# Optimization experiments

Hardware: AMD Instinct MI355X
Metric: run time of the kernel (lower is better)

## Reference

```python
import jax, jax.numpy as jnp
import numpy as np

N = 100000
E = 1600000
IN_C = 256
HID = 256
OUT_C = 10
G = 64  # number of graphs in batch


def setup_inputs() -> dict:
    key = jax.random.key(0)
    k1, k2, k3, k4, k5, k6, k7 = jax.random.split(key, 7)
    x = jax.random.normal(k1, (N, IN_C), dtype=jnp.float32)
    edge_index = jax.random.randint(k2, (2, E), 0, N, dtype=jnp.int64)
    batch = jnp.sort(jax.random.randint(k3, (N,), 0, G, dtype=jnp.int64))
    # GCNConv weight (glorot-ish) and bias
    W1 = jax.random.normal(k4, (IN_C, HID), dtype=jnp.float32) / np.sqrt(IN_C)
    b1 = jnp.zeros((HID,), dtype=jnp.float32)
    # final Linear
    W2 = jax.random.normal(k5, (HID, OUT_C), dtype=jnp.float32) / np.sqrt(HID)
    b2 = jax.random.normal(k6, (OUT_C,), dtype=jnp.float32) * 0.01
    return {"x": x, "edge_index": edge_index, "batch": batch,
            "W1": W1, "b1": b1, "W2": W2, "b2": b2}


def reference(x, edge_index, batch, W1, b1, W2, b2):
    # ---- GCNConv(in_channels, hidden_dim), add_self_loops=True, symmetric norm ----
    src = edge_index[0]
    dst = edge_index[1]
    loop = jnp.arange(N, dtype=src.dtype)
    src = jnp.concatenate([src, loop])  # [E+N]
    dst = jnp.concatenate([dst, loop])
    # degree on destination nodes (incl. self-loops) -> >= 1 everywhere
    deg = jax.ops.segment_sum(jnp.ones_like(dst, dtype=x.dtype), dst, num_segments=N)
    dinv = jax.lax.rsqrt(deg)  # deg >= 1, safe
    h = x @ W1  # linear transform first (PyG GCNConv order)
    norm = dinv[src] * dinv[dst]  # [E+N]
    msgs = h[src] * norm[:, None]  # gather + scale
    agg = jax.ops.segment_sum(msgs, dst, num_segments=N) + b1  # scatter-add + bias
    # ---- relu; dropout is identity in eval mode ----
    hrelu = jax.nn.relu(agg)
    # ---- global_mean_pool over batch ids ----
    sums = jax.ops.segment_sum(hrelu, batch, num_segments=G)
    counts = jax.ops.segment_sum(jnp.ones((N,), dtype=x.dtype), batch, num_segments=G)
    pooled = sums / jnp.maximum(counts, 1.0)[:, None]  # [G, HID]
    # ---- final linear ----
    return pooled @ W2 + b2
```

## Files before the change

### kernel.cpp

```cpp
#include <hip/hip_runtime.h>

#define NN 100000
#define EE 1600000
#define C 256
#define OUTC 10
#define NG 64

#define BSH 7
#define NBK 782
#define CHUNK 2048
#define NBLK1 ((EE + CHUNK - 1) / CHUNK)
#define PADSLACK 1024

#define NODES_PER_GROUP 8
#define NODES_PER_BLOCK 32
#define AGG_BLOCKS 3125
#define AGG_HALF 1563

#define PRE_CNT_BLKS 391
#define PRE_W1_BLKS 256

typedef __bf16 bf16x8 __attribute__((ext_vector_type(8)));
typedef float f32x4 __attribute__((ext_vector_type(4)));
typedef float f32x2 __attribute__((ext_vector_type(2)));

__device__ __forceinline__ int chan_logical(int p) {
    return ((p & 15) << 4) | (p >> 4);
}

__device__ __forceinline__ ushort f2bf(float f) {
    unsigned u = __float_as_uint(f);
    return (ushort)((u + 0x7fffu + ((u >> 16) & 1u)) >> 16);
}
__device__ __forceinline__ bf16x8 as_bf16x8(uint4 v) {
    union { uint4 u; bf16x8 b; } c; c.u = v; return c.b;
}

__device__ __forceinline__ void acc_fp8x4(float4& s, unsigned v) {
    f32x2 lo = __builtin_amdgcn_cvt_pk_f32_fp8(v, false);
    f32x2 hi = __builtin_amdgcn_cvt_pk_f32_fp8(v, true);
    s.x += lo[0]; s.y += lo[1]; s.z += hi[0]; s.w += hi[1];
}

__global__ __launch_bounds__(256) void pre_kernel(const int* __restrict__ ei,
                                                  int* __restrict__ bhist,
                                                  const int* __restrict__ batch,
                                                  float* __restrict__ cnt,
                                                  const float* __restrict__ W1,
                                                  ushort* __restrict__ w1f,
                                                  unsigned* __restrict__ gz) {
    __shared__ int h[NBK];
    const int bid = blockIdx.x;
    const int t = threadIdx.x;
    if (bid < NBLK1) {
        for (int i = t; i < NBK; i += 256) h[i] = 0;
        __syncthreads();
        const int base = bid * CHUNK;
        const int end = min(base + CHUNK, EE);
        for (int e = base + t; e < end; e += 256)
            atomicAdd(&h[ei[EE + e] >> BSH], 1);
        __syncthreads();
        for (int i = t; i < NBK; i += 256)
            if (h[i]) atomicAdd(&bhist[i], h[i]);
    } else if (bid < NBLK1 + PRE_CNT_BLKS) {
        if (t < NG) h[t] = 0;
        __syncthreads();
        int i = (bid - NBLK1) * 256 + t;
        if (i < NN) atomicAdd(&h[batch[i]], 1);
        __syncthreads();
        if (t < NG && h[t]) atomicAdd(&cnt[t], (float)h[t]);
    } else {
        int wb = bid - (NBLK1 + PRE_CNT_BLKS);
        int tt = wb * 256 + t;
        if (wb == 0 && t < 64) gz[t] = 0;
        int k = tt >> 8, n = tt & 255;
        int kb = k >> 5, q = (k >> 3) & 3, j = k & 7;
        int nt = n >> 4, ln = (n & 15) + q * 16;
        w1f[(size_t)(((kb * 16 + nt) * 64) + ln) * 8 + j] = f2bf(W1[tt]);
    }
}

__global__ __launch_bounds__(1024) void bucket_scan_kernel(const int* __restrict__ bhist,
                                                           int* __restrict__ bbase,
                                                           int* __restrict__ bcur) {
    __shared__ int sc[1024];
    const int t = threadIdx.x;
    int v = (t < NBK) ? bhist[t] : 0;
    sc[t] = v;
    __syncthreads();
    for (int off = 1; off < 1024; off <<= 1) {
        int tmp = (t >= off) ? sc[t - off] : 0;
        __syncthreads();
        sc[t] += tmp;
        __syncthreads();
    }
    int excl = sc[t] - v;
    if (t < NBK) { bbase[t] = excl; bcur[t] = excl; }
    if (t == NBK - 1) bbase[NBK] = sc[t];
}

__global__ __launch_bounds__(256) void bucket_scatter_kernel(const int* __restrict__ ei,
                                                             int* __restrict__ bcur,
                                                             unsigned* __restrict__ bmaj) {
    __shared__ int h[NBK];
    for (int t = threadIdx.x; t < NBK; t += 256) h[t] = 0;
    __syncthreads();
    const int base = blockIdx.x * CHUNK;
    const int end = min(base + CHUNK, EE);
    for (int e = base + threadIdx.x; e < end; e += 256)
        atomicAdd(&h[ei[EE + e] >> BSH], 1);
    __syncthreads();
    for (int t = threadIdx.x; t < NBK; t += 256) {
        int c = h[t];
        h[t] = c ? atomicAdd(&bcur[t], c) : 0;
    }
    __syncthreads();
    for (int e = base + threadIdx.x; e < end; e += 256) {
        int d = ei[EE + e];
        int s = ei[e];
        int b = d >> BSH;
        int p = atomicAdd(&h[b], 1);
        bmaj[p] = (unsigned)s | ((unsigned)(d & 127) << 17);
    }
}

__global__ __launch_bounds__(256) void bucket_csr_kernel(const unsigned* __restrict__ bmaj,
                                                         const int* __restrict__ bbase,
                                                         int* __restrict__ rowend,
                                                         float* __restrict__ dinv,
                                                         int* __restrict__ csrcol) {
    __shared__ int h[128];
    __shared__ int sc[128];
    __shared__ int cur[128];
    const int b = blockIdx.x;
    const int t = threadIdx.x;
    const int e0 = bbase[b], e1 = bbase[b + 1];
    const int region0 = ((e0 + 7) & ~7) + b * PADSLACK;
    if (t < 128) h[t] = 0;
    __syncthreads();
    for (int e = e0 + t; e < e1; e += 256)
        atomicAdd(&h[bmaj[e] >> 17], 1);
    __syncthreads();
    int deg = 0, pd = 0, node = 0;
    if (t < 128) {
        deg = h[t];
        node = b * 128 + t;
        pd = (node < NN) ? ((deg + 7) & ~7) : 0;
        sc[t] = pd;
    }
    __syncthreads();
    for (int off = 1; off < 128; off <<= 1) {
        int tmp = (t >= off && t < 128) ? sc[t - off] : 0;
        __syncthreads();
        if (t < 128) sc[t] += tmp;
        __syncthreads();
    }
    if (t < 128) {
        int pstart = region0 + sc[t] - pd;
        if (node < NN) {
            rowend[node] = pstart + pd;
            dinv[node] = rsqrtf((float)deg + 1.0f);
            for (int j = deg; j < pd; j++) csrcol[pstart + j] = NN;
        }
        cur[t] = pstart;
    }
    __syncthreads();
    for (int e = e0 + t; e < e1; e += 256) {
        unsigned v = bmaj[e];
        int p = atomicAdd(&cur[v >> 17], 1);
        csrcol[p] = (int)(v & 0x1FFFFu);
    }
}

__global__ __launch_bounds__(256, 2) void gemm_mfma_kernel(const float* __restrict__ x,
                                                           const ushort* __restrict__ w1f,
                                                           const float* __restrict__ dinv,
                                                           uchar* __restrict__ g) {
    const int lane = threadIdx.x & 63;
    const int wid = threadIdx.x >> 6;
    const int wave = blockIdx.x * 4 + wid;
    const int r0 = wave * 32;
    if (r0 >= NN) return;
    const int mrow = lane & 15;
    const int q = lane >> 4;

    f32x4 acc[2][16];
    #pragma unroll
    for (int mt = 0; mt < 2; mt++)
        #pragma unroll
        for (int nt = 0; nt < 16; nt++)
            acc[mt][nt] = (f32x4){0.f, 0.f, 0.f, 0.f};

    const float* xp0 = x + (size_t)(r0 + mrow) * C + q * 8;
    const float* xp1 = xp0 + (size_t)16 * C;
    const ushort* bp = w1f + (size_t)lane * 8;

    #pragma unroll 1
    for (int kb = 0; kb < 8; kb++) {
        const int ko = kb * 32;
        float4 a0lo = *(const float4*)(xp0 + ko);
        float4 a0hi = *(const float4*)(xp0 + ko + 4);
        float4 a1lo = *(const float4*)(xp1 + ko);
        float4 a1hi = *(const float4*)(xp1 + ko + 4);
        uint4 bbv[16];
        const ushort* bkb = bp + (size_t)kb * 16 * 512;
        #pragma unroll
        for (int nt = 0; nt < 16; nt++)
            bbv[nt] = *(const uint4*)(bkb + (size_t)nt * 512);

        bf16x8 a0, a1;
        a0[0] = (__bf16)a0lo.x; a0[1] = (__bf16)a0lo.y;
        a0[2] = (__bf16)a0lo.z; a0[3] = (__bf16)a0lo.w;
        a0[4] = (__bf16)a0hi.x; a0[5] = (__bf16)a0hi.y;
        a0[6] = (__bf16)a0hi.z; a0[7] = (__bf16)a0hi.w;
        a1[0] = (__bf16)a1lo.x; a1[1] = (__bf16)a1lo.y;
        a1[2] = (__bf16)a1lo.z; a1[3] = (__bf16)a1lo.w;
        a1[4] = (__bf16)a1hi.x; a1[5] = (__bf16)a1hi.y;
        a1[6] = (__bf16)a1hi.z; a1[7] = (__bf16)a1hi.w;

        #pragma unroll
        for (int nt = 0; nt < 16; nt++) {
            bf16x8 bb = as_bf16x8(bbv[nt]);
            acc[0][nt] = __builtin_amdgcn_mfma_f32_16x16x32_bf16(a0, bb, acc[0][nt], 0, 0, 0);
            acc[1][nt] = __builtin_amdgcn_mfma_f32_16x16x32_bf16(a1, bb, acc[1][nt], 0, 0, 0);
        }
    }

    #pragma unroll
    for (int mt = 0; mt < 2; mt++) {
        #pragma unroll
        for (int r = 0; r < 4; r++) {
            int row = r0 + mt * 16 + q * 4 + r;
            float dv = dinv[row];
            uint4 dw;
            unsigned t0, t1, t2, t3;
            t0 = __builtin_amdgcn_cvt_pk_fp8_f32(acc[mt][0][r] * dv,  acc[mt][1][r] * dv,  0,  false);
            dw.x = __builtin_amdgcn_cvt_pk_fp8_f32(acc[mt][2][r] * dv,  acc[mt][3][r] * dv,  t0, true);
            t1 = __builtin_amdgcn_cvt_pk_fp8_f32(acc[mt][4][r] * dv,  acc[mt][5][r] * dv,  0,  false);
            dw.y = __builtin_amdgcn_cvt_pk_fp8_f32(acc[mt][6][r] * dv,  acc[mt][7][r] * dv,  t1, true);
            t2 = __builtin_amdgcn_cvt_pk_fp8_f32(acc[mt][8][r] * dv,  acc[mt][9][r] * dv,  0,  false);
            dw.z = __builtin_amdgcn_cvt_pk_fp8_f32(acc[mt][10][r] * dv, acc[mt][11][r] * dv, t2, true);
            t3 = __builtin_amdgcn_cvt_pk_fp8_f32(acc[mt][12][r] * dv, acc[mt][13][r] * dv, 0,  false);
            dw.w = __builtin_amdgcn_cvt_pk_fp8_f32(acc[mt][14][r] * dv, acc[mt][15][r] * dv, t3, true);
            *(uint4*)(g + (size_t)row * C + mrow * 16) = dw;
        }
    }
}

__global__ __launch_bounds__(256) void agg_pool_kernel(const unsigned* __restrict__ g32,
                                                       const int* __restrict__ rowend,
                                                       const int* __restrict__ csrcol,
                                                       const int* __restrict__ bbase,
                                                       const float* __restrict__ dinv,
                                                       const float* __restrict__ b1,
                                                       const int* __restrict__ batch,
                                                       float* __restrict__ sums,
                                                       const int blk0) {
    const int lane = threadIdx.x & 63;
    const int wid = threadIdx.x >> 6;
    const int c4 = lane * 4;
    const int nodeA = (blockIdx.x + blk0) * NODES_PER_BLOCK + wid * NODES_PER_GROUP;
    float4 bv;
    bv.x = b1[chan_logical(c4 + 0)];
    bv.y = b1[chan_logical(c4 + 1)];
    bv.z = b1[chan_logical(c4 + 2)];
    bv.w = b1[chan_logical(c4 + 3)];
    const unsigned* gp = g32 + lane;

    int rprev;
    if ((nodeA & 127) == 0) {
        int b = nodeA >> BSH;
        rprev = ((bbase[b] + 7) & ~7) + b * PADSLACK;
    } else {
        rprev = rowend[nodeA - 1];
    }

    float4 pool = make_float4(0.f, 0.f, 0.f, 0.f);
    int curb = -1;
    #pragma unroll 1
    for (int i = nodeA; i < nodeA + NODES_PER_GROUP; i++) {
        int r1 = rowend[i];
        int r0 = rprev;
        rprev = r1;
        int bi = batch[i];
        if (bi != curb) {
            if (curb >= 0) {
                atomicAdd(&sums[curb * C + c4 + 0], pool.x);
                atomicAdd(&sums[curb * C + c4 + 1], pool.y);
                atomicAdd(&sums[curb * C + c4 + 2], pool.z);
                atomicAdd(&sums[curb * C + c4 + 3], pool.w);
            }
            curb = bi;
            pool = make_float4(0.f, 0.f, 0.f, 0.f);
        }
        float4 s = make_float4(0.f, 0.f, 0.f, 0.f);
        acc_fp8x4(s, gp[(size_t)i * 64]);
        #pragma unroll 1
        for (int e = r0; e < r1; e += 8) {
            int4 iv0 = *(const int4*)(csrcol + e);
            int4 iv1 = *(const int4*)(csrcol + e + 4);
            unsigned v0 = gp[(size_t)iv0.x * 64];
            unsigned v1 = gp[(size_t)iv0.y * 64];
            unsigned v2 = gp[(size_t)iv0.z * 64];
            unsigned v3 = gp[(size_t)iv0.w * 64];
            unsigned v4 = gp[(size_t)iv1.x * 64];
            unsigned v5 = gp[(size_t)iv1.y * 64];
            unsigned v6 = gp[(size_t)iv1.z * 64];
            unsigned v7 = gp[(size_t)iv1.w * 64];
            acc_fp8x4(s, v0); acc_fp8x4(s, v1); acc_fp8x4(s, v2); acc_fp8x4(s, v3);
            acc_fp8x4(s, v4); acc_fp8x4(s, v5); acc_fp8x4(s, v6); acc_fp8x4(s, v7);
        }
        float dv = dinv[i];
        pool.x += fmaxf(fmaf(dv, s.x, bv.x), 0.f);
        pool.y += fmaxf(fmaf(dv, s.y, bv.y), 0.f);
        pool.z += fmaxf(fmaf(dv, s.z, bv.z), 0.f);
        pool.w += fmaxf(fmaf(dv, s.w, bv.w), 0.f);
    }
    if (curb >= 0) {
        atomicAdd(&sums[curb * C + c4 + 0], pool.x);
        atomicAdd(&sums[curb * C + c4 + 1], pool.y);
        atomicAdd(&sums[curb * C + c4 + 2], pool.z);
        atomicAdd(&sums[curb * C + c4 + 3], pool.w);
    }
}

__global__ __launch_bounds__(256) void final_kernel(const float* __restrict__ sums,
                                                    const float* __restrict__ cnt,
                                                    const float* __restrict__ W2,
                                                    const float* __restrict__ b2,
                                                    float* __restrict__ out) {
    __shared__ float p[C];
    int gi = blockIdx.x;
    float cdiv = fmaxf(cnt[gi], 1.0f);
    p[threadIdx.x] = sums[gi * C + threadIdx.x] / cdiv;
    __syncthreads();
    if (threadIdx.x < OUTC) {
        float acc = b2[threadIdx.x];
        for (int k = 0; k < C; k++)
            acc += p[k] * W2[chan_logical(k) * OUTC + threadIdx.x];
        out[gi * OUTC + threadIdx.x] = acc;
    }
}

extern "C" void kernel_launch(void* const* d_in, const int* in_sizes, int n_in,
                              void* d_out, int out_size, void* d_ws, size_t ws_size,
                              hipStream_t stream) {
    const float* x     = (const float*)d_in[0];
    const int*   ei    = (const int*)d_in[1];
    const int*   batch = (const int*)d_in[2];
    const float* W1    = (const float*)d_in[3];
    const float* b1    = (const float*)d_in[4];
    const float* W2    = (const float*)d_in[5];
    const float* b2    = (const float*)d_in[6];
    float* out = (float*)d_out;

    char* w = (char*)d_ws;
    size_t off = 0;
    auto carve = [&](size_t bytes) {
        void* p = w + off;
        off = (off + bytes + 255) & ~(size_t)255;
        return p;
    };
    uchar*    g        = (uchar*)   carve((size_t)(NN + 1) * C);
    int*      rowend   = (int*)     carve((size_t)NN * 4);
    float*    dinv     = (float*)   carve((size_t)NN * 4);
    int*      csrcol   = (int*)     carve((size_t)(EE + (size_t)NBK * PADSLACK + 128) * 4);
    unsigned* bmaj     = (unsigned*)carve((size_t)EE * 4);
    int*      bbase    = (int*)     carve((size_t)(NBK + 1) * 4);
    int*      bcur     = (int*)     carve((size_t)NBK * 4);
    ushort*   w1f      = (ushort*)  carve((size_t)C * C * 2);
    int*      bhist    = (int*)     carve((size_t)NBK * 4);
    float*    sums     = (float*)   carve((size_t)NG * C * 4);
    float*    cnt      = (float*)   carve((size_t)NG * 4);
    size_t zero_bytes = (size_t)((char*)cnt + (size_t)NG * 4 - (char*)bhist);

    hipMemsetAsync(bhist, 0, zero_bytes, stream);

    pre_kernel<<<NBLK1 + PRE_CNT_BLKS + PRE_W1_BLKS, 256, 0, stream>>>(
        ei, bhist, batch, cnt, W1, w1f, (unsigned*)(g + (size_t)NN * C));
    bucket_scan_kernel<<<1, 1024, 0, stream>>>(bhist, bbase, bcur);
    bucket_scatter_kernel<<<NBLK1, 256, 0, stream>>>(ei, bcur, bmaj);
    bucket_csr_kernel<<<NBK, 256, 0, stream>>>(bmaj, bbase, rowend, dinv, csrcol);
    gemm_mfma_kernel<<<(NN / 32 + 3) / 4, 256, 0, stream>>>(x, w1f, dinv, g);
    agg_pool_kernel<<<AGG_HALF, 256, 0, stream>>>(
        (const unsigned*)g, rowend, csrcol, bbase, dinv, b1, batch, sums, 0);
    agg_pool_kernel<<<AGG_BLOCKS - AGG_HALF, 256, 0, stream>>>(
        (const unsigned*)g, rowend, csrcol, bbase, dinv, b1, batch, sums, AGG_HALF);
    final_kernel<<<NG, 256, 0, stream>>>(sums, cnt, W2, b2, out);
}
```

Before: 409.1 us.

## Replace two-level bucket sort CSR build with global degree count and atomic scatter

The CSR build no longer runs a bucket histogram, a bucket-major scatter and a per-bucket CSR pass. It now counts per-node degrees with global atomics, reduces and scans padded degrees per 256-node bucket, assigns row starts, and scatters edges straight into csrcol with per-node atomic cursors. This drops the intermediate bmaj array and one pass over the edges, at the cost of heavily contended global atomics and nondeterministic order within each row. The aggregation launch is also split into four launches instead of two.

```diff
diff --git a/kernel.cpp b/kernel.cpp
--- a/kernel.cpp
+++ b/kernel.cpp
@@ -6,16 +6,16 @@
 #define OUTC 10
 #define NG 64
 
-#define BSH 7
-#define NBK 782
-#define CHUNK 2048
-#define NBLK1 ((EE + CHUNK - 1) / CHUNK)
-#define PADSLACK 1024
+#define BSH 8
+#define NBK 391
+
+#define E4 (EE / 4)
+#define EBLK ((E4 + 255) / 256)
 
 #define NODES_PER_GROUP 8
 #define NODES_PER_BLOCK 32
 #define AGG_BLOCKS 3125
-#define AGG_HALF 1563
+#define AGG_Q 782
 
 #define PRE_CNT_BLKS 391
 #define PRE_W1_BLKS 256
@@ -43,34 +43,33 @@
 }
 
 __global__ __launch_bounds__(256) void pre_kernel(const int* __restrict__ ei,
-                                                  int* __restrict__ bhist,
+                                                  int* __restrict__ degcur,
                                                   const int* __restrict__ batch,
                                                   float* __restrict__ cnt,
                                                   const float* __restrict__ W1,
                                                   ushort* __restrict__ w1f,
                                                   unsigned* __restrict__ gz) {
-    __shared__ int h[NBK];
+    __shared__ int h[NG];
     const int bid = blockIdx.x;
     const int t = threadIdx.x;
-    if (bid < NBLK1) {
-        for (int i = t; i < NBK; i += 256) h[i] = 0;
-        __syncthreads();
-        const int base = bid * CHUNK;
-        const int end = min(base + CHUNK, EE);
-        for (int e = base + t; e < end; e += 256)
-            atomicAdd(&h[ei[EE + e] >> BSH], 1);
-        __syncthreads();
-        for (int i = t; i < NBK; i += 256)
-            if (h[i]) atomicAdd(&bhist[i], h[i]);
-    } else if (bid < NBLK1 + PRE_CNT_BLKS) {
+    if (bid < EBLK) {
+        int idx = bid * 256 + t;
+        if (idx < E4) {
+            int4 d4 = ((const int4*)(ei + EE))[idx];
+            atomicAdd(&degcur[d4.x], 1);
+            atomicAdd(&degcur[d4.y], 1);
+            atomicAdd(&degcur[d4.z], 1);
+            atomicAdd(&degcur[d4.w], 1);
+        }
+    } else if (bid < EBLK + PRE_CNT_BLKS) {
         if (t < NG) h[t] = 0;
         __syncthreads();
-        int i = (bid - NBLK1) * 256 + t;
+        int i = (bid - EBLK) * 256 + t;
         if (i < NN) atomicAdd(&h[batch[i]], 1);
         __syncthreads();
         if (t < NG && h[t]) atomicAdd(&cnt[t], (float)h[t]);
     } else {
-        int wb = bid - (NBLK1 + PRE_CNT_BLKS);
+        int wb = bid - (EBLK + PRE_CNT_BLKS);
         int tt = wb * 256 + t;
         if (wb == 0 && t < 64) gz[t] = 0;
         int k = tt >> 8, n = tt & 255;
@@ -80,96 +79,78 @@
     }
 }
 
-__global__ __launch_bounds__(1024) void bucket_scan_kernel(const int* __restrict__ bhist,
-                                                           int* __restrict__ bbase,
-                                                           int* __restrict__ bcur) {
-    __shared__ int sc[1024];
+__global__ __launch_bounds__(256) void bsum_kernel(const int* __restrict__ degcur,
+                                                   int* __restrict__ bsum) {
+    __shared__ int r[256];
+    const int b = blockIdx.x;
     const int t = threadIdx.x;
-    int v = (t < NBK) ? bhist[t] : 0;
+    int node = b * 256 + t;
+    int d = (node < NN) ? degcur[node] : 0;
+    r[t] = (d + 7) & ~7;
+    __syncthreads();
+    for (int off = 128; off > 0; off >>= 1) {
+        if (t < off) r[t] += r[t + off];
+        __syncthreads();
+    }
+    if (t == 0) bsum[b] = r[0];
+}
+
+__global__ __launch_bounds__(512) void bucket_scan_kernel(const int* __restrict__ bsum,
+                                                          int* __restrict__ bbase) {
+    __shared__ int sc[512];
+    const int t = threadIdx.x;
+    int v = (t < NBK) ? bsum[t] : 0;
     sc[t] = v;
     __syncthreads();
-    for (int off = 1; off < 1024; off <<= 1) {
+    for (int off = 1; off < 512; off <<= 1) {
         int tmp = (t >= off) ? sc[t - off] : 0;
         __syncthreads();
         sc[t] += tmp;
         __syncthreads();
     }
-    int excl = sc[t] - v;
-    if (t < NBK) { bbase[t] = excl; bcur[t] = excl; }
+    if (t < NBK) bbase[t] = sc[t] - v;
     if (t == NBK - 1) bbase[NBK] = sc[t];
 }
 
-__global__ __launch_bounds__(256) void bucket_scatter_kernel(const int* __restrict__ ei,
-                                                             int* __restrict__ bcur,
-                                                             unsigned* __restrict__ bmaj) {
-    __shared__ int h[NBK];
-    for (int t = threadIdx.x; t < NBK; t += 256) h[t] = 0;
-    __syncthreads();
-    const int base = blockIdx.x * CHUNK;
-    const int end = min(base + CHUNK, EE);
-    for (int e = base + threadIdx.x; e < end; e += 256)
-        atomicAdd(&h[ei[EE + e] >> BSH], 1);
-    __syncthreads();
-    for (int t = threadIdx.x; t < NBK; t += 256) {
-        int c = h[t];
-        h[t] = c ? atomicAdd(&bcur[t], c) : 0;
-    }
-    __syncthreads();
-    for (int e = base + threadIdx.x; e < end; e += 256) {
-        int d = ei[EE + e];
-        int s = ei[e];
-        int b = d >> BSH;
-        int p = atomicAdd(&h[b], 1);
-        bmaj[p] = (unsigned)s | ((unsigned)(d & 127) << 17);
-    }
-}
-
-__global__ __launch_bounds__(256) void bucket_csr_kernel(const unsigned* __restrict__ bmaj,
-                                                         const int* __restrict__ bbase,
-                                                         int* __restrict__ rowend,
-                                                         float* __restrict__ dinv,
-                                                         int* __restrict__ csrcol) {
-    __shared__ int h[128];
-    __shared__ int sc[128];
-    __shared__ int cur[128];
+__global__ __launch_bounds__(256) void csrlite_kernel(int* __restrict__ degcur,
+                                                      const int* __restrict__ bbase,
+                                                      int* __restrict__ rowend,
+                                                      float* __restrict__ dinv,
+                                                      int* __restrict__ csrcol) {
+    __shared__ int sc[256];
     const int b = blockIdx.x;
     const int t = threadIdx.x;
-    const int e0 = bbase[b], e1 = bbase[b + 1];
-    const int region0 = ((e0 + 7) & ~7) + b * PADSLACK;
-    if (t < 128) h[t] = 0;
+    int node = b * 256 + t;
+    int d = (node < NN) ? degcur[node] : 0;
+    int pd = (node < NN) ? ((d + 7) & ~7) : 0;
+    sc[t] = pd;
     __syncthreads();
-    for (int e = e0 + t; e < e1; e += 256)
-        atomicAdd(&h[bmaj[e] >> 17], 1);
-    __syncthreads();
-    int deg = 0, pd = 0, node = 0;
-    if (t < 128) {
-        deg = h[t];
-        node = b * 128 + t;
-        pd = (node < NN) ? ((deg + 7) & ~7) : 0;
-        sc[t] = pd;
-    }
-    __syncthreads();
-    for (int off = 1; off < 128; off <<= 1) {
-        int tmp = (t >= off && t < 128) ? sc[t - off] : 0;
-        __syncthreads();
-        if (t < 128) sc[t] += tmp;
-        __syncthreads();
-    }
-    if (t < 128) {
-        int pstart = region0 + sc[t] - pd;
-        if (node < NN) {
-            rowend[node] = pstart + pd;
-            dinv[node] = rsqrtf((float)deg + 1.0f);
-            for (int j = deg; j < pd; j++) csrcol[pstart + j] = NN;
-        }
-        cur[t] = pstart;
-    }
-    __syncthreads();
-    for (int e = e0 + t; e < e1; e += 256) {
-        unsigned v = bmaj[e];
-        int p = atomicAdd(&cur[v >> 17], 1);
-        csrcol[p] = (int)(v & 0x1FFFFu);
-    }
+    for (int off = 1; off < 256; off <<= 1) {
+        int tmp = (t >= off) ? sc[t - off] : 0;
+        __syncthreads();
+        sc[t] += tmp;
+        __syncthreads();
+    }
+    if (node < NN) {
+        int pstart = bbase[b] + sc[t] - pd;
+        rowend[node] = pstart + pd;
+        dinv[node] = rsqrtf((float)d + 1.0f);
+        for (int j = d; j < pd; j++) csrcol[pstart + j] = NN;
+        degcur[node] = pstart;
+    }
+}
+
+__global__ __launch_bounds__(256) void scatter_kernel(const int* __restrict__ ei,
+                                                      int* __restrict__ cur,
+                                                      int* __restrict__ csrcol) {
+    int idx = blockIdx.x * 256 + threadIdx.x;
+    if (idx >= E4) return;
+    int4 s4 = ((const int4*)ei)[idx];
+    int4 d4 = ((const int4*)(ei + EE))[idx];
+    int p0 = atomicAdd(&cur[d4.x], 1); csrcol[p0] = s4.x;
+    int p1 = atomicAdd(&cur[d4.y], 1); csrcol[p1] = s4.y;
+    int p2 = atomicAdd(&cur[d4.z], 1); csrcol[p2] = s4.z;
+    int p3 = atomicAdd(&cur[d4.w], 1); csrcol[p3] = s4.w;
 }
 
 __global__ __launch_bounds__(256, 2) void gemm_mfma_kernel(const float* __restrict__ x,
@@ -268,9 +249,8 @@
     const unsigned* gp = g32 + lane;
 
     int rprev;
-    if ((nodeA & 127) == 0) {
-        int b = nodeA >> BSH;
-        rprev = ((bbase[b] + 7) & ~7) + b * PADSLACK;
+    if ((nodeA & 255) == 0) {
+        rprev = bbase[nodeA >> BSH];
     } else {
         rprev = rowend[nodeA - 1];
     }
@@ -364,27 +344,31 @@
     uchar*    g        = (uchar*)   carve((size_t)(NN + 1) * C);
     int*      rowend   = (int*)     carve((size_t)NN * 4);
     float*    dinv     = (float*)   carve((size_t)NN * 4);
-    int*      csrcol   = (int*)     carve((size_t)(EE + (size_t)NBK * PADSLACK + 128) * 4);
-    unsigned* bmaj     = (unsigned*)carve((size_t)EE * 4);
+    int*      csrcol   = (int*)     carve((size_t)(EE + 8 * NN + 64) * 4);
+    int*      bsum     = (int*)     carve((size_t)NBK * 4);
     int*      bbase    = (int*)     carve((size_t)(NBK + 1) * 4);
-    int*      bcur     = (int*)     carve((size_t)NBK * 4);
     ushort*   w1f      = (ushort*)  carve((size_t)C * C * 2);
-    int*      bhist    = (int*)     carve((size_t)NBK * 4);
+    int*      degcur   = (int*)     carve((size_t)NN * 4);
     float*    sums     = (float*)   carve((size_t)NG * C * 4);
     float*    cnt      = (float*)   carve((size_t)NG * 4);
-    size_t zero_bytes = (size_t)((char*)cnt + (size_t)NG * 4 - (char*)bhist);
-
-    hipMemsetAsync(bhist, 0, zero_bytes, stream);
-
-    pre_kernel<<<NBLK1 + PRE_CNT_BLKS + PRE_W1_BLKS, 256, 0, stream>>>(
-        ei, bhist, batch, cnt, W1, w1f, (unsigned*)(g + (size_t)NN * C));
-    bucket_scan_kernel<<<1, 1024, 0, stream>>>(bhist, bbase, bcur);
-    bucket_scatter_kernel<<<NBLK1, 256, 0, stream>>>(ei, bcur, bmaj);
-    bucket_csr_kernel<<<NBK, 256, 0, stream>>>(bmaj, bbase, rowend, dinv, csrcol);
+    size_t zero_bytes = (size_t)((char*)cnt + (size_t)NG * 4 - (char*)degcur);
+
+    hipMemsetAsync(degcur, 0, zero_bytes, stream);
+
+    pre_kernel<<<EBLK + PRE_CNT_BLKS + PRE_W1_BLKS, 256, 0, stream>>>(
+        ei, degcur, batch, cnt, W1, w1f, (unsigned*)(g + (size_t)NN * C));
+    bsum_kernel<<<NBK, 256, 0, stream>>>(degcur, bsum);
+    bucket_scan_kernel<<<1, 512, 0, stream>>>(bsum, bbase);
+    csrlite_kernel<<<NBK, 256, 0, stream>>>(degcur, bbase, rowend, dinv, csrcol);
+    scatter_kernel<<<EBLK, 256, 0, stream>>>(ei, degcur, csrcol);
     gemm_mfma_kernel<<<(NN / 32 + 3) / 4, 256, 0, stream>>>(x, w1f, dinv, g);
-    agg_pool_kernel<<<AGG_HALF, 256, 0, stream>>>(
+    agg_pool_kernel<<<AGG_Q, 256, 0, stream>>>(
         (const unsigned*)g, rowend, csrcol, bbase, dinv, b1, batch, sums, 0);
-    agg_pool_kernel<<<AGG_BLOCKS - AGG_HALF, 256, 0, stream>>>(
-        (const unsigned*)g, rowend, csrcol, bbase, dinv, b1, batch, sums, AGG_HALF);
+    agg_pool_kernel<<<AGG_Q, 256, 0, stream>>>(
+        (const unsigned*)g, rowend, csrcol, bbase, dinv, b1, batch, sums, AGG_Q);
+    agg_pool_kernel<<<AGG_Q, 256, 0, stream>>>(
+        (const unsigned*)g, rowend, csrcol, bbase, dinv, b1, batch, sums, 2 * AGG_Q);
+    agg_pool_kernel<<<AGG_BLOCKS - 3 * AGG_Q, 256, 0, stream>>>(
+        (const unsigned*)g, rowend, csrcol, bbase, dinv, b1, batch, sums, 3 * AGG_Q);
     final_kernel<<<NG, 256, 0, stream>>>(sums, cnt, W2, b2, out);
 }
```

New measurement: 610.5 us. 1.49x slower.

## Replace atomic bucket cursors with per-chunk histograms and a column prefix scan

Applied to the files above, without the earlier changes.

The edge bucketing now stores a per-chunk histogram and computes each chunk's per-bucket offset with a new column-scan kernel. This removes the scatter kernel's second histogram pass and its global atomics on bucket cursors, and makes the scatter deterministic. Edge loads become int4 vector loads with a larger chunk size, and the aggregation launch is split into four pieces instead of two. The cost is an extra kernel launch and a strided 391x782 histogram read and write, while the scatter now runs with half as many blocks.

```diff
diff --git a/kernel.cpp b/kernel.cpp
--- a/kernel.cpp
+++ b/kernel.cpp
@@ -8,14 +8,16 @@
 
 #define BSH 7
 #define NBK 782
-#define CHUNK 2048
-#define NBLK1 ((EE + CHUNK - 1) / CHUNK)
+#define CHUNK 4096
+#define NCHUNK 391
+#define CI4 1024
+#define E4 (EE / 4)
 #define PADSLACK 1024
 
 #define NODES_PER_GROUP 8
 #define NODES_PER_BLOCK 32
 #define AGG_BLOCKS 3125
-#define AGG_HALF 1563
+#define AGG_Q 782
 
 #define PRE_CNT_BLKS 391
 #define PRE_W1_BLKS 256
@@ -43,7 +45,7 @@
 }
 
 __global__ __launch_bounds__(256) void pre_kernel(const int* __restrict__ ei,
-                                                  int* __restrict__ bhist,
+                                                  int* __restrict__ chunkhist,
                                                   const int* __restrict__ batch,
                                                   float* __restrict__ cnt,
                                                   const float* __restrict__ W1,
@@ -52,25 +54,30 @@
     __shared__ int h[NBK];
     const int bid = blockIdx.x;
     const int t = threadIdx.x;
-    if (bid < NBLK1) {
+    if (bid < NCHUNK) {
         for (int i = t; i < NBK; i += 256) h[i] = 0;
         __syncthreads();
-        const int base = bid * CHUNK;
-        const int end = min(base + CHUNK, EE);
-        for (int e = base + t; e < end; e += 256)
-            atomicAdd(&h[ei[EE + e] >> BSH], 1);
+        const int base4 = bid * CI4;
+        const int end4 = min(base4 + CI4, E4);
+        for (int i = base4 + t; i < end4; i += 256) {
+            int4 d4 = ((const int4*)(ei + EE))[i];
+            atomicAdd(&h[d4.x >> BSH], 1);
+            atomicAdd(&h[d4.y >> BSH], 1);
+            atomicAdd(&h[d4.z >> BSH], 1);
+            atomicAdd(&h[d4.w >> BSH], 1);
+        }
         __syncthreads();
         for (int i = t; i < NBK; i += 256)
-            if (h[i]) atomicAdd(&bhist[i], h[i]);
-    } else if (bid < NBLK1 + PRE_CNT_BLKS) {
+            chunkhist[bid * NBK + i] = h[i];
+    } else if (bid < NCHUNK + PRE_CNT_BLKS) {
         if (t < NG) h[t] = 0;
         __syncthreads();
-        int i = (bid - NBLK1) * 256 + t;
+        int i = (bid - NCHUNK) * 256 + t;
         if (i < NN) atomicAdd(&h[batch[i]], 1);
         __syncthreads();
         if (t < NG && h[t]) atomicAdd(&cnt[t], (float)h[t]);
     } else {
-        int wb = bid - (NBLK1 + PRE_CNT_BLKS);
+        int wb = bid - (NCHUNK + PRE_CNT_BLKS);
         int tt = wb * 256 + t;
         if (wb == 0 && t < 64) gz[t] = 0;
         int k = tt >> 8, n = tt & 255;
@@ -80,12 +87,29 @@
     }
 }
 
-__global__ __launch_bounds__(1024) void bucket_scan_kernel(const int* __restrict__ bhist,
-                                                           int* __restrict__ bbase,
-                                                           int* __restrict__ bcur) {
+__global__ __launch_bounds__(512) void rowscan_kernel(int* __restrict__ chunkhist,
+                                                      int* __restrict__ bsum) {
+    __shared__ int sc[512];
+    const int b = blockIdx.x;
+    const int t = threadIdx.x;
+    int v = (t < NCHUNK) ? chunkhist[t * NBK + b] : 0;
+    sc[t] = v;
+    __syncthreads();
+    for (int off = 1; off < 512; off <<= 1) {
+        int tmp = (t >= off) ? sc[t - off] : 0;
+        __syncthreads();
+        sc[t] += tmp;
+        __syncthreads();
+    }
+    if (t < NCHUNK) chunkhist[t * NBK + b] = sc[t] - v;
+    if (t == 511) bsum[b] = sc[511];
+}
+
+__global__ __launch_bounds__(1024) void bucket_scan_kernel(const int* __restrict__ bsum,
+                                                           int* __restrict__ bbase) {
     __shared__ int sc[1024];
     const int t = threadIdx.x;
-    int v = (t < NBK) ? bhist[t] : 0;
+    int v = (t < NBK) ? bsum[t] : 0;
     sc[t] = v;
     __syncthreads();
     for (int off = 1; off < 1024; off <<= 1) {
@@ -94,33 +118,33 @@
         sc[t] += tmp;
         __syncthreads();
     }
-    int excl = sc[t] - v;
-    if (t < NBK) { bbase[t] = excl; bcur[t] = excl; }
+    if (t < NBK) bbase[t] = sc[t] - v;
     if (t == NBK - 1) bbase[NBK] = sc[t];
 }
 
 __global__ __launch_bounds__(256) void bucket_scatter_kernel(const int* __restrict__ ei,
-                                                             int* __restrict__ bcur,
+                                                             const int* __restrict__ chunkhist,
+                                                             const int* __restrict__ bbase,
                                                              unsigned* __restrict__ bmaj) {
-    __shared__ int h[NBK];
-    for (int t = threadIdx.x; t < NBK; t += 256) h[t] = 0;
-    __syncthreads();
-    const int base = blockIdx.x * CHUNK;
-    const int end = min(base + CHUNK, EE);
-    for (int e = base + threadIdx.x; e < end; e += 256)
-        atomicAdd(&h[ei[EE + e] >> BSH], 1);
-    __syncthreads();
-    for (int t = threadIdx.x; t < NBK; t += 256) {
-        int c = h[t];
-        h[t] = c ? atomicAdd(&bcur[t], c) : 0;
-    }
-    __syncthreads();
-    for (int e = base + threadIdx.x; e < end; e += 256) {
-        int d = ei[EE + e];
-        int s = ei[e];
-        int b = d >> BSH;
-        int p = atomicAdd(&h[b], 1);
-        bmaj[p] = (unsigned)s | ((unsigned)(d & 127) << 17);
+    __shared__ int cur[NBK];
+    const int c = blockIdx.x;
+    const int t = threadIdx.x;
+    for (int b = t; b < NBK; b += 256)
+        cur[b] = bbase[b] + chunkhist[c * NBK + b];
+    __syncthreads();
+    const int base4 = c * CI4;
+    const int end4 = min(base4 + CI4, E4);
+    for (int i = base4 + t; i < end4; i += 256) {
+        int4 s4 = ((const int4*)ei)[i];
+        int4 d4 = ((const int4*)(ei + EE))[i];
+        int p0 = atomicAdd(&cur[d4.x >> BSH], 1);
+        bmaj[p0] = (unsigned)s4.x | ((unsigned)(d4.x & 127) << 17);
+        int p1 = atomicAdd(&cur[d4.y >> BSH], 1);
+        bmaj[p1] = (unsigned)s4.y | ((unsigned)(d4.y & 127) << 17);
+        int p2 = atomicAdd(&cur[d4.z >> BSH], 1);
+        bmaj[p2] = (unsigned)s4.z | ((unsigned)(d4.z & 127) << 17);
+        int p3 = atomicAdd(&cur[d4.w >> BSH], 1);
+        bmaj[p3] = (unsigned)s4.w | ((unsigned)(d4.w & 127) << 17);
     }
 }
 
@@ -366,25 +390,30 @@
     float*    dinv     = (float*)   carve((size_t)NN * 4);
     int*      csrcol   = (int*)     carve((size_t)(EE + (size_t)NBK * PADSLACK + 128) * 4);
     unsigned* bmaj     = (unsigned*)carve((size_t)EE * 4);
+    int*      chunkhist= (int*)     carve((size_t)NCHUNK * NBK * 4);
+    int*      bsum     = (int*)     carve((size_t)NBK * 4);
     int*      bbase    = (int*)     carve((size_t)(NBK + 1) * 4);
-    int*      bcur     = (int*)     carve((size_t)NBK * 4);
     ushort*   w1f      = (ushort*)  carve((size_t)C * C * 2);
-    int*      bhist    = (int*)     carve((size_t)NBK * 4);
     float*    sums     = (float*)   carve((size_t)NG * C * 4);
     float*    cnt      = (float*)   carve((size_t)NG * 4);
-    size_t zero_bytes = (size_t)((char*)cnt + (size_t)NG * 4 - (char*)bhist);
-
-    hipMemsetAsync(bhist, 0, zero_bytes, stream);
-
-    pre_kernel<<<NBLK1 + PRE_CNT_BLKS + PRE_W1_BLKS, 256, 0, stream>>>(
-        ei, bhist, batch, cnt, W1, w1f, (unsigned*)(g + (size_t)NN * C));
-    bucket_scan_kernel<<<1, 1024, 0, stream>>>(bhist, bbase, bcur);
-    bucket_scatter_kernel<<<NBLK1, 256, 0, stream>>>(ei, bcur, bmaj);
+    size_t zero_bytes = (size_t)((char*)cnt + (size_t)NG * 4 - (char*)sums);
+
+    hipMemsetAsync(sums, 0, zero_bytes, stream);
+
+    pre_kernel<<<NCHUNK + PRE_CNT_BLKS + PRE_W1_BLKS, 256, 0, stream>>>(
+        ei, chunkhist, batch, cnt, W1, w1f, (unsigned*)(g + (size_t)NN * C));
+    rowscan_kernel<<<NBK, 512, 0, stream>>>(chunkhist, bsum);
+    bucket_scan_kernel<<<1, 1024, 0, stream>>>(bsum, bbase);
+    bucket_scatter_kernel<<<NCHUNK, 256, 0, stream>>>(ei, chunkhist, bbase, bmaj);
     bucket_csr_kernel<<<NBK, 256, 0, stream>>>(bmaj, bbase, rowend, dinv, csrcol);
     gemm_mfma_kernel<<<(NN / 32 + 3) / 4, 256, 0, stream>>>(x, w1f, dinv, g);
-    agg_pool_kernel<<<AGG_HALF, 256, 0, stream>>>(
+    agg_pool_kernel<<<AGG_Q, 256, 0, stream>>>(
         (const unsigned*)g, rowend, csrcol, bbase, dinv, b1, batch, sums, 0);
-    agg_pool_kernel<<<AGG_BLOCKS - AGG_HALF, 256, 0, stream>>>(
-        (const unsigned*)g, rowend, csrcol, bbase, dinv, b1, batch, sums, AGG_HALF);
+    agg_pool_kernel<<<AGG_Q, 256, 0, stream>>>(
+        (const unsigned*)g, rowend, csrcol, bbase, dinv, b1, batch, sums, AGG_Q);
+    agg_pool_kernel<<<AGG_Q, 256, 0, stream>>>(
+        (const unsigned*)g, rowend, csrcol, bbase, dinv, b1, batch, sums, 2 * AGG_Q);
+    agg_pool_kernel<<<AGG_BLOCKS - 3 * AGG_Q, 256, 0, stream>>>(
+        (const unsigned*)g, rowend, csrcol, bbase, dinv, b1, batch, sums, 3 * AGG_Q);
     final_kernel<<<NG, 256, 0, stream>>>(sums, cnt, W2, b2, out);
 }
```

Measured after the change: 459.0 us. +12.2%, slower.
